# Performance work log

Measured on AMD Instinct MI355X. Metric: run time of the kernel, lower is better.

## Reference

```python
import jax, jax.numpy as jnp
import numpy as np

GAMMA = 0.5
EPS = 1e-06
REL_THRESH = 1e-09


def setup_inputs() -> dict:
    key = jax.random.key(0)
    k1, k2 = jax.random.split(key)
    B, T, D = 4, 4096, 256
    A_rel = jax.random.uniform(k1, (B, T, T), dtype=jnp.float32)
    # symmetrize as the docstring states A_rel is symmetric
    A_rel = 0.5 * (A_rel + jnp.swapaxes(A_rel, -1, -2))
    k_seq = jax.random.normal(k2, (B, T, D), dtype=jnp.float32)
    return {"A_rel": A_rel, "k_seq": k_seq}


def reference(A_rel, k_seq):
    # init_sequence: symmetric normalization W = D^{-1/2} A D^{-1/2}
    D = jnp.sum(A_rel, axis=-1) + EPS                  # (B, T)
    d_inv_sqrt = 1.0 / jnp.sqrt(D)                     # (B, T)
    W = A_rel * d_inv_sqrt[:, :, None] * d_inv_sqrt[:, None, :]  # (B, T, T)

    T = A_rel.shape[1]
    # step t uses W[:, t, :t+1] -> lower-triangular (incl. diagonal) causal mask
    tril = jnp.tril(jnp.ones((T, T), dtype=W.dtype))   # (T, T)
    W_causal = W * tril                                # (B, T, T)

    # a_t = sum_{s<=t} W[b,t,s] * k_s  for every t at once
    a = jnp.einsum('bts,bsd->btd', W_causal, k_seq)    # (B, T, D)

    # has_relation[b,t] = max_{s<=t} |W[b,t,s]| > 1e-9
    has_relation = jnp.max(jnp.abs(W) * tril, axis=-1) > REL_THRESH  # (B, T)

    a_scaled = a * jnp.sqrt(jnp.asarray(GAMMA, dtype=a.dtype))
    out = a_scaled * has_relation[:, :, None].astype(a_scaled.dtype)
    return out
```

## Files before the change

kernel.cpp:

```cpp
#include <hip/hip_runtime.h>
#include <hip/hip_bf16.h>

constexpr int Bn = 4;
constexpr int Tn = 4096;
constexpr int Dn = 256;
constexpr int NT = Tn / 64;
constexpr int NTRI = NT * (NT + 1) / 2;

using ushort = unsigned short;
typedef short short8 __attribute__((ext_vector_type(8)));
typedef float f32x4 __attribute__((ext_vector_type(4)));

__device__ __forceinline__ ushort f2bu(float f) {
    __hip_bfloat16 h = __float2bfloat16(f);
    return __builtin_bit_cast(unsigned short, h);
}
__device__ __forceinline__ void gld_lds16(const ushort* g, ushort* l) {
    __builtin_amdgcn_global_load_lds((const __attribute__((address_space(1))) void*)g,
                                     (__attribute__((address_space(3))) void*)l,
                                     16, 0, 0);
}

__global__ __launch_bounds__(256) void rowsum_convert_kernel(
    const float* __restrict__ A, float* __restrict__ dis, ushort* __restrict__ Apk) {
    int r = blockIdx.x;
    int b = r >> 12;
    int t = r & (Tn - 1);
    int it = t >> 6, m = t & 63;
    const float* row = A + (size_t)r * Tn;
    ushort* tb = Apk + (size_t)b * NTRI * 4096 + (size_t)(it * (it + 1) / 2) * 4096 + m * 64;
    int tid = threadIdx.x;
    float s = 0.f;
#pragma unroll
    for (int q = 0; q < 2; ++q) {
        int g = q * 256 + tid;
        int c0 = g * 8;
        float4 v0 = *(const float4*)(row + c0);
        float4 v1 = *(const float4*)(row + c0 + 4);
        s += v0.x + v0.y + v0.z + v0.w + v1.x + v1.y + v1.z + v1.w;
        int kt = g >> 3;
        if (kt <= it) {
            float f[8] = {v0.x, v0.y, v0.z, v0.w, v1.x, v1.y, v1.z, v1.w};
            int c = c0 & 63;
            if (kt == it) {
#pragma unroll
                for (int j = 0; j < 8; ++j)
                    if (c + j > m) f[j] = 0.f;
            }
            unsigned w[4];
#pragma unroll
            for (int e = 0; e < 4; ++e)
                w[e] = (unsigned)f2bu(f[2 * e]) | ((unsigned)f2bu(f[2 * e + 1]) << 16);
            *(uint4*)(tb + (size_t)kt * 4096 + c) = make_uint4(w[0], w[1], w[2], w[3]);
        }
    }
#pragma unroll
    for (int k = 1; k < 64; k <<= 1) s += __shfl_xor(s, k, 64);
    __shared__ float ws[4];
    if ((tid & 63) == 0) ws[tid >> 6] = s;
    __syncthreads();
    if (tid == 0) {
        float tot = ws[0] + ws[1] + ws[2] + ws[3];
        dis[r] = rsqrtf(tot + 1e-6f);
    }
}

__global__ __launch_bounds__(256) void scale_transpose_kernel(
    const float* __restrict__ K, const float* __restrict__ dis, ushort* __restrict__ kT) {
    int bid = blockIdx.x;
    int b = bid >> 8;
    int rr = bid & 255;
    int st = rr >> 2, dt = rr & 3;
    int s0 = st * 64, d0 = dt * 64;
    __shared__ ushort tile[64][72];
    int tid = threadIdx.x;
#pragma unroll
    for (int q = 0; q < 2; ++q) {
        int idx = q * 256 + tid;
        int sl = idx >> 3, dl0 = (idx & 7) * 8;
        const float* g = K + ((size_t)(b * Tn + s0 + sl) * Dn + d0 + dl0);
        float sc = dis[b * Tn + s0 + sl];
        float4 v0 = *(const float4*)g;
        float4 v1 = *(const float4*)(g + 4);
        tile[sl][dl0 + 0] = f2bu(v0.x * sc);
        tile[sl][dl0 + 1] = f2bu(v0.y * sc);
        tile[sl][dl0 + 2] = f2bu(v0.z * sc);
        tile[sl][dl0 + 3] = f2bu(v0.w * sc);
        tile[sl][dl0 + 4] = f2bu(v1.x * sc);
        tile[sl][dl0 + 5] = f2bu(v1.y * sc);
        tile[sl][dl0 + 6] = f2bu(v1.z * sc);
        tile[sl][dl0 + 7] = f2bu(v1.w * sc);
    }
    __syncthreads();
#pragma unroll
    for (int q = 0; q < 2; ++q) {
        int idx = q * 256 + tid;
        int dl = idx >> 3, sl0 = (idx & 7) * 8;
        unsigned w[4];
#pragma unroll
        for (int e = 0; e < 4; ++e) {
            unsigned lo = tile[sl0 + 2 * e][dl];
            unsigned hi = tile[sl0 + 2 * e + 1][dl];
            w[e] = lo | (hi << 16);
        }
        *(uint4*)(kT + ((size_t)(b * Dn + d0 + dl) * Tn + s0 + sl0)) =
            make_uint4(w[0], w[1], w[2], w[3]);
    }
}

constexpr int BK = 64;

__global__ __launch_bounds__(256) void gemm_causal_kernel(
    const ushort* __restrict__ Apk, const ushort* __restrict__ kT,
    const float* __restrict__ dis, float* __restrict__ out) {
    __shared__ __attribute__((aligned(16))) ushort As[2][64 * BK];
    __shared__ __attribute__((aligned(16))) ushort Bs[2][64 * BK];
    __shared__ float rs[64];

    int bid = blockIdx.x;
    int it = 63 - (bid >> 4);
    int sub = bid & 15;
    int b = sub >> 2;
    int d0 = (sub & 3) * 64;
    int t0 = it * 64;

    int tid = threadIdx.x;
    int lane = tid & 63;
    int w = tid >> 6;
    int l15 = lane & 15;
    int kq = (lane >> 4) * 8;

    const ushort* Atri = Apk + (size_t)b * NTRI * 4096 + (size_t)(it * (it + 1) / 2) * 4096;
    const size_t kTbase = (size_t)(b * Dn + d0) * Tn;

    if (tid < 64) rs[tid] = 0.70710678118654752f * dis[b * Tn + t0 + tid];

    f32x4 acc[2][2];
#pragma unroll
    for (int mi = 0; mi < 2; ++mi)
#pragma unroll
        for (int ni = 0; ni < 2; ++ni) acc[mi][ni] = (f32x4){0.f, 0.f, 0.f, 0.f};

    int mrow = (w >> 1) * 32;
    int ncol = (w & 1) * 32;
    int nkt = it + 1;

    auto stage = [&](int buf, int kt) {
#pragma unroll
        for (int q = 0; q < 2; ++q) {
            int idx = q * 256 + tid;
            gld_lds16(Atri + (size_t)kt * 4096 + idx * 8, &As[buf][idx * 8]);
        }
#pragma unroll
        for (int q = 0; q < 2; ++q) {
            int idx = q * 256 + tid;
            int n = idx >> 3, sc = (idx & 7) * 8;
            gld_lds16(kT + kTbase + (size_t)n * Tn + kt * BK + sc, &Bs[buf][idx * 8]);
        }
    };

    stage(0, 0);
    __syncthreads();

    for (int kt = 0; kt < nkt; ++kt) {
        int cur = kt & 1;
        if (kt + 1 < nkt) stage(cur ^ 1, kt + 1);
#pragma unroll
        for (int ki = 0; ki < 2; ++ki) {
            int kc = ki * 32 + kq;
            short8 af[2];
#pragma unroll
            for (int mi = 0; mi < 2; ++mi)
                af[mi] = *(const short8*)&As[cur][(mrow + 16 * mi + l15) * BK + kc];
            short8 bfr[2];
#pragma unroll
            for (int ni = 0; ni < 2; ++ni)
                bfr[ni] = *(const short8*)&Bs[cur][(ncol + 16 * ni + l15) * BK + kc];
#pragma unroll
            for (int mi = 0; mi < 2; ++mi)
#pragma unroll
                for (int ni = 0; ni < 2; ++ni)
                    acc[mi][ni] = __builtin_amdgcn_mfma_f32_16x16x32_bf16(
                        af[mi], bfr[ni], acc[mi][ni], 0, 0, 0);
        }
        __syncthreads();
    }

#pragma unroll
    for (int mi = 0; mi < 2; ++mi) {
#pragma unroll
        for (int ni = 0; ni < 2; ++ni) {
            int tl = mrow + 16 * mi + (lane >> 4) * 4;
            int d = d0 + ncol + 16 * ni + l15;
#pragma unroll
            for (int r = 0; r < 4; ++r) {
                int t = t0 + tl + r;
                out[(size_t)(b * Tn + t) * Dn + d] = acc[mi][ni][r] * rs[tl + r];
            }
        }
    }
}

extern "C" void kernel_launch(void* const* d_in, const int* in_sizes, int n_in,
                              void* d_out, int out_size, void* d_ws, size_t ws_size,
                              hipStream_t stream) {
    const float* A = (const float*)d_in[0];
    const float* K = (const float*)d_in[1];
    float* out = (float*)d_out;

    float* dis = (float*)d_ws;
    ushort* kT = (ushort*)(dis + Bn * Tn);
    ushort* Apk = kT + (size_t)Bn * Dn * Tn;

    rowsum_convert_kernel<<<dim3(Bn * Tn), dim3(256), 0, stream>>>(A, dis, Apk);
    scale_transpose_kernel<<<dim3(Bn * (Tn / 64) * (Dn / 64)), dim3(256), 0, stream>>>(K, dis, kT);
    gemm_causal_kernel<<<dim3(NT * 16), dim3(256), 0, stream>>>(Apk, kT, dis, out);
}
```

Baseline: 448.8 us.

## Read only lower triangle of A, using symmetry for row sums via column atomics

The old row-sum pass read every element of the full TxT matrix A. The new pass reads only the lower-triangular 64x64 tiles. Each tile adds its row sums to its own rows and, relying on A being symmetric, its column sums to the mirrored rows through atomic adds. Diagonal tiles are counted only once. This roughly halves the HBM reads of A, the dominant traffic. The cost is a memset, a small extra kernel, atomics and floating-point sums that are no longer deterministic. It is correct only because the input is symmetric, which the task states.

```diff
diff --git a/kernel.cpp b/kernel.cpp
--- a/kernel.cpp
+++ b/kernel.cpp
@@ -21,48 +21,72 @@
                                      16, 0, 0);
 }
 
-__global__ __launch_bounds__(256) void rowsum_convert_kernel(
-    const float* __restrict__ A, float* __restrict__ dis, ushort* __restrict__ Apk) {
-    int r = blockIdx.x;
-    int b = r >> 12;
-    int t = r & (Tn - 1);
-    int it = t >> 6, m = t & 63;
-    const float* row = A + (size_t)r * Tn;
-    ushort* tb = Apk + (size_t)b * NTRI * 4096 + (size_t)(it * (it + 1) / 2) * 4096 + m * 64;
+__global__ __launch_bounds__(256) void tri_pass_kernel(
+    const float* __restrict__ A, float* __restrict__ acc, ushort* __restrict__ Apk) {
+    __shared__ float tile[64][68];
+    int bid = blockIdx.x;
+    int b = bid / NTRI;
+    int r = bid - b * NTRI;
+    int it = (int)((sqrtf(8.f * r + 1.f) - 1.f) * 0.5f);
+    while ((it + 1) * (it + 2) / 2 <= r) ++it;
+    while (it * (it + 1) / 2 > r) --it;
+    int kt = r - it * (it + 1) / 2;
+    int t0 = it * 64, s0 = kt * 64;
+    bool diag = (kt == it);
+
     int tid = threadIdx.x;
-    float s = 0.f;
-#pragma unroll
-    for (int q = 0; q < 2; ++q) {
-        int g = q * 256 + tid;
-        int c0 = g * 8;
-        float4 v0 = *(const float4*)(row + c0);
-        float4 v1 = *(const float4*)(row + c0 + 4);
-        s += v0.x + v0.y + v0.z + v0.w + v1.x + v1.y + v1.z + v1.w;
-        int kt = g >> 3;
-        if (kt <= it) {
-            float f[8] = {v0.x, v0.y, v0.z, v0.w, v1.x, v1.y, v1.z, v1.w};
-            int c = c0 & 63;
-            if (kt == it) {
-#pragma unroll
-                for (int j = 0; j < 8; ++j)
-                    if (c + j > m) f[j] = 0.f;
-            }
-            unsigned w[4];
-#pragma unroll
-            for (int e = 0; e < 4; ++e)
-                w[e] = (unsigned)f2bu(f[2 * e]) | ((unsigned)f2bu(f[2 * e + 1]) << 16);
-            *(uint4*)(tb + (size_t)kt * 4096 + c) = make_uint4(w[0], w[1], w[2], w[3]);
-        }
-    }
-#pragma unroll
-    for (int k = 1; k < 64; k <<= 1) s += __shfl_xor(s, k, 64);
-    __shared__ float ws[4];
-    if ((tid & 63) == 0) ws[tid >> 6] = s;
-    __syncthreads();
-    if (tid == 0) {
-        float tot = ws[0] + ws[1] + ws[2] + ws[3];
-        dis[r] = rsqrtf(tot + 1e-6f);
-    }
+    int i = tid >> 2;
+    int c0 = (tid & 3) * 16;
+
+    const float* g = A + ((size_t)(b * Tn + t0 + i) * Tn + s0 + c0);
+    float4 v[4];
+#pragma unroll
+    for (int q = 0; q < 4; ++q) v[q] = *(const float4*)(g + 4 * q);
+
+    float f[16];
+#pragma unroll
+    for (int q = 0; q < 4; ++q) {
+        f[4 * q + 0] = v[q].x; f[4 * q + 1] = v[q].y;
+        f[4 * q + 2] = v[q].z; f[4 * q + 3] = v[q].w;
+    }
+    float rp = 0.f;
+#pragma unroll
+    for (int e = 0; e < 16; ++e) rp += f[e];
+    rp += __shfl_xor(rp, 1, 64);
+    rp += __shfl_xor(rp, 2, 64);
+    if ((tid & 3) == 0) atomicAdd(&acc[b * Tn + t0 + i], rp);
+
+#pragma unroll
+    for (int q = 0; q < 4; ++q) *(float4*)&tile[i][c0 + 4 * q] = v[q];
+
+    ushort* tb = Apk + (size_t)b * NTRI * 4096 + (size_t)(it * (it + 1) / 2 + kt) * 4096;
+    unsigned w[8];
+#pragma unroll
+    for (int e = 0; e < 8; ++e) {
+        float lo = f[2 * e], hi = f[2 * e + 1];
+        if (diag) {
+            if (c0 + 2 * e > i)     lo = 0.f;
+            if (c0 + 2 * e + 1 > i) hi = 0.f;
+        }
+        w[e] = (unsigned)f2bu(lo) | ((unsigned)f2bu(hi) << 16);
+    }
+    *(uint4*)(tb + i * 64 + c0)     = make_uint4(w[0], w[1], w[2], w[3]);
+    *(uint4*)(tb + i * 64 + c0 + 8) = make_uint4(w[4], w[5], w[6], w[7]);
+
+    if (!diag) {
+        __syncthreads();
+        int j = tid & 63, p = tid >> 6;
+        float cp = 0.f;
+#pragma unroll
+        for (int q = 0; q < 16; ++q) cp += tile[p * 16 + q][j];
+        atomicAdd(&acc[b * Tn + s0 + j], cp);
+    }
+}
+
+__global__ __launch_bounds__(256) void dis_kernel(const float* __restrict__ acc,
+                                                  float* __restrict__ dis) {
+    int r = blockIdx.x * 256 + threadIdx.x;
+    dis[r] = rsqrtf(acc[r] + 1e-6f);
 }
 
 __global__ __launch_bounds__(256) void scale_transpose_kernel(
@@ -208,11 +232,14 @@
     const float* K = (const float*)d_in[1];
     float* out = (float*)d_out;
 
-    float* dis = (float*)d_ws;
+    float* acc = (float*)d_ws;
+    float* dis = acc + Bn * Tn;
     ushort* kT = (ushort*)(dis + Bn * Tn);
     ushort* Apk = kT + (size_t)Bn * Dn * Tn;
 
-    rowsum_convert_kernel<<<dim3(Bn * Tn), dim3(256), 0, stream>>>(A, dis, Apk);
+    hipMemsetAsync(acc, 0, Bn * Tn * sizeof(float), stream);
+    tri_pass_kernel<<<dim3(Bn * NTRI), dim3(256), 0, stream>>>(A, acc, Apk);
+    dis_kernel<<<dim3(Bn * Tn / 256), dim3(256), 0, stream>>>(acc, dis);
     scale_transpose_kernel<<<dim3(Bn * (Tn / 64) * (Dn / 64)), dim3(256), 0, stream>>>(K, dis, kT);
     gemm_causal_kernel<<<dim3(NT * 16), dim3(256), 0, stream>>>(Apk, kT, dis, out);
 }
```

After: 401.8 us. -10.5%, faster.
